# Performance work log

Hardware: AMD Instinct MI355X
Metric: run time of the kernel (lower is better)

Reference implementation:

```python
import jax, jax.numpy as jnp
import numpy as np

N_USERS = 100000
N_ITEMS = 100000
D = 64
B, P, H = 32, 1000, 128
EPS = 1e-12


def setup_inputs() -> dict:
    key = jax.random.key(0)
    ks = jax.random.split(key, 9)
    user_index = jax.random.randint(ks[0], (B,), 0, N_USERS)
    pred_item_indices = jax.random.randint(ks[1], (B, P), 0, N_ITEMS)
    history_item_indices = jax.random.randint(ks[2], (B, H), 0, N_ITEMS)
    # positive listen-time gaps (seconds-scale)
    history_timedeltas = jax.random.uniform(ks[3], (B, H), jnp.float32) * 100.0
    history_weights = jnp.ones((B, H), jnp.float32)
    embedding_user = jax.random.normal(ks[4], (N_USERS + 1, D), jnp.float32) * 0.1
    embedding_item = jax.random.normal(ks[5], (N_ITEMS + 1, D), jnp.float32) * 0.1
    user_lamb = jax.random.normal(ks[6], (N_USERS + 1, 1), jnp.float32) * 0.01
    user_bias = jax.random.normal(ks[7], (N_USERS + 1, 1), jnp.float32) * 0.01
    item_bias = jax.random.normal(ks[8], (N_ITEMS + 1, 1), jnp.float32) * 0.01
    return {
        'user_index': user_index,
        'pred_item_indices': pred_item_indices,
        'history_item_indices': history_item_indices,
        'history_timedeltas': history_timedeltas,
        'history_weights': history_weights,
        'embedding_user': embedding_user,
        'embedding_item': embedding_item,
        'user_lamb': user_lamb,
        'user_bias': user_bias,
        'item_bias': item_bias,
        'global_lamb': jnp.float32(1.0),
        'alpha': jnp.float32(1.0),
        'beta': jnp.float32(-0.065),
        'gamma': jnp.float32(0.5),
        'cutoff': jnp.float32(3.0),
        'smooth': jnp.float32(1.0),
        'force': jnp.float32(1.0),
    }


def reference(user_index, pred_item_indices, history_item_indices,
              history_timedeltas, history_weights,
              embedding_user, embedding_item, user_lamb, user_bias, item_bias,
              global_lamb, alpha, beta, gamma, cutoff, smooth, force):
    u = embedding_user[user_index][:, None, :]              # [B,1,D]
    p = embedding_item[pred_item_indices]                   # [B,P,D]
    dist_ui = jnp.sqrt(jnp.sum((u - p) ** 2, axis=2) + EPS)  # [B,P]

    h = embedding_item[history_item_indices]                # [B,H,D]
    # pairwise L2 via Gram trick: avoids the [B,H,P,D] broadcast intermediate
    sq = (jnp.sum(h * h, -1)[:, :, None]
          + jnp.sum(p * p, -1)[:, None, :]
          - 2.0 * jnp.einsum('bhd,bpd->bhp', h, p))         # [B,H,P]
    dist = jnp.sqrt(jnp.maximum(sq, 0.0) + EPS)

    denom = jax.nn.sigmoid(smooth - force * smooth)
    kern = jax.nn.sigmoid(smooth / (1.0 + dist) - force * smooth) / denom  # [B,H,P]

    td = (history_timedeltas + cutoff) ** (-0.5) * history_weights  # [B,H]
    lamb = global_lamb + user_lamb[user_index]              # [B,1]
    res = lamb * jnp.einsum('bh,bhp->bp', td, kern)         # [B,P]

    out = jnp.maximum(0.0, dist_ui - res)                   # [B,P]
    I = (alpha * out + beta * out ** 2 + gamma
         + user_bias[user_index]                            # [B,1] broadcast
         + item_bias[pred_item_indices][..., 0])            # [B,P]
    return I
```

## Files before the change

kernel.cpp:

```cpp
#include <hip/hip_runtime.h>
#include <hip/hip_bf16.h>

#define EPS 1e-12f

constexpr int B = 32, P = 1000, H = 128, D = 64;
constexpr int PT = 128;
constexpr int TILB = 8;
constexpr int NT = 512;

typedef __attribute__((ext_vector_type(8))) short bf16x8;
typedef __attribute__((ext_vector_type(4))) float f32x4;

__device__ __forceinline__ float fast_rcp(float x)  { return __builtin_amdgcn_rcpf(x); }
__device__ __forceinline__ float fast_sqrt(float x) { return __builtin_amdgcn_sqrtf(x); }

__device__ __forceinline__ int pk2(float x, float y) {
    union { __hip_bfloat162 t; int i; } u;
    u.t = __float22bfloat162_rn(make_float2(x, y));
    return u.i;
}
__device__ __forceinline__ bf16x8 cvt8(f32x4 a, f32x4 b) {
    union { bf16x8 v; int i[4]; } u;
    u.i[0] = pk2(a.x, a.y); u.i[1] = pk2(a.z, a.w);
    u.i[2] = pk2(b.x, b.y); u.i[3] = pk2(b.z, b.w);
    return u.v;
}
__device__ __forceinline__ f32x4 scale4(f32x4 v, float s) {
    f32x4 r; r.x = v.x * s; r.y = v.y * s; r.z = v.z * s; r.w = v.w * s;
    return r;
}
__device__ __forceinline__ float sumsq16(f32x4 a, f32x4 b, f32x4 c, f32x4 d) {
    return (a.x*a.x + a.y*a.y + a.z*a.z + a.w*a.w)
         + (b.x*b.x + b.y*b.y + b.z*b.z + b.w*b.w)
         + (c.x*c.x + c.y*c.y + c.z*c.z + c.w*c.w)
         + (d.x*d.x + d.y*d.y + d.z*d.z + d.w*d.w);
}

__device__ __forceinline__ int swz(int row, int kg) { return kg ^ ((row >> 1) & 3); }

__global__ __launch_bounds__(NT, 2)
void ex2vec_kernel(const int* __restrict__ user_index,
                   const int* __restrict__ pred_items,
                   const int* __restrict__ hist_items,
                   const float* __restrict__ hist_td,
                   const float* __restrict__ hist_w,
                   const float* __restrict__ emb_user,
                   const float* __restrict__ emb_item,
                   const float* __restrict__ user_lamb,
                   const float* __restrict__ user_bias,
                   const float* __restrict__ item_bias,
                   const float* __restrict__ sc_global_lamb,
                   const float* __restrict__ sc_alpha,
                   const float* __restrict__ sc_beta,
                   const float* __restrict__ sc_gamma,
                   const float* __restrict__ sc_cutoff,
                   const float* __restrict__ sc_smooth,
                   const float* __restrict__ sc_force,
                   float* __restrict__ out)
{
    __shared__ bf16x8 afs[2][H][4];
    __shared__ float  hh[H];
    __shared__ float  tds[H];

    const int b    = blockIdx.x >> 3;
    const int tile = blockIdx.x & 7;
    const int tid  = threadIdx.x;
    const int w    = tid >> 6;
    const int lane = tid & 63;
    const int col  = lane & 15;
    const int kg   = lane >> 4;

    const int pg   = tile * PT + w * 16 + col;
    const int pgc  = pg < P ? pg : P - 1;
    const int pidx = pred_items[b * P + pgc];

    const float* prow = emb_item + (size_t)pidx * D + kg * 8;
    const f32x4 p0 = *(const f32x4*)(prow);
    const f32x4 p1 = *(const f32x4*)(prow + 4);
    const f32x4 p2 = *(const f32x4*)(prow + 32);
    const f32x4 p3 = *(const f32x4*)(prow + 36);

    const float cutoff = *sc_cutoff;

    {
        const int r = tid >> 2;
        const int q = tid & 3;
        const int hidx = hist_items[b * H + r];
        const f32x4* hsrc = (const f32x4*)(emb_item + (size_t)hidx * D + q * 16);
        const f32x4 v0 = hsrc[0], v1 = hsrc[1], v2 = hsrc[2], v3 = hsrc[3];

        float s = sumsq16(v0, v1, v2, v3);
        s += __shfl_xor(s, 1);
        s += __shfl_xor(s, 2);
        if (q == 0) {
            hh[r]  = s;
            tds[r] = hist_w[b * H + r] * __frsqrt_rn(hist_td[b * H + r] + cutoff);
        }
        afs[q >> 1][r][swz(r, (q & 1) * 2)]     = cvt8(v0, v1);
        afs[q >> 1][r][swz(r, (q & 1) * 2 + 1)] = cvt8(v2, v3);
    }

    float pp = sumsq16(p0, p1, p2, p3);
    pp += __shfl_xor(pp, 16);
    pp += __shfl_xor(pp, 32);
    const bf16x8 bfr0 = cvt8(scale4(p0, -2.f), scale4(p1, -2.f));
    const bf16x8 bfr1 = cvt8(scale4(p2, -2.f), scale4(p3, -2.f));

    const float smooth = *sc_smooth;
    const float fs     = *sc_force * smooth;

    __syncthreads();

    float pres = 0.f;
    #pragma unroll
    for (int t = 0; t < 8; ++t) {
        const int row = t * 16 + col;
        const bf16x8 af0 = afs[0][row][swz(row, kg)];
        const bf16x8 af1 = afs[1][row][swz(row, kg)];
        const f32x4  hh4 = *(const f32x4*)(hh  + t * 16 + kg * 4);
        const f32x4  td4 = *(const f32x4*)(tds + t * 16 + kg * 4);

        f32x4 acc;
        acc.x = pp + hh4[0]; acc.y = pp + hh4[1];
        acc.z = pp + hh4[2]; acc.w = pp + hh4[3];
        acc = __builtin_amdgcn_mfma_f32_16x16x32_bf16(af0, bfr0, acc, 0, 0, 0);
        acc = __builtin_amdgcn_mfma_f32_16x16x32_bf16(af1, bfr1, acc, 0, 0, 0);

        #pragma unroll
        for (int j = 0; j < 4; ++j) {
            const float dist = fast_sqrt(fmaxf(acc[j], 0.f) + EPS);
            const float x    = smooth * fast_rcp(1.f + dist) - fs;
            pres += td4[j] * fast_rcp(1.f + __expf(-x));
        }
    }
    pres += __shfl_xor(pres, 16);
    pres += __shfl_xor(pres, 32);

    const int uidx = user_index[b];
    const float* urow = emb_user + (size_t)uidx * D + kg * 8;
    f32x4 d0 = *(const f32x4*)(urow)      - p0;
    f32x4 d1 = *(const f32x4*)(urow + 4)  - p1;
    f32x4 d2 = *(const f32x4*)(urow + 32) - p2;
    f32x4 d3 = *(const f32x4*)(urow + 36) - p3;
    float dp = sumsq16(d0, d1, d2, d3);
    dp += __shfl_xor(dp, 16);
    dp += __shfl_xor(dp, 32);

    if (lane < 16 && pg < P) {
        const float inv_denom = 1.f + __expf(fs - smooth);
        const float lamb      = (*sc_global_lamb + user_lamb[uidx]) * inv_denom;
        const float dist_ui   = fast_sqrt(dp + EPS);
        const float o = fmaxf(0.f, dist_ui - lamb * pres);
        out[b * P + pg] = (*sc_alpha) * o + (*sc_beta) * o * o + (*sc_gamma)
                          + user_bias[uidx] + item_bias[pidx];
    }
}

extern "C" void kernel_launch(void* const* d_in, const int* in_sizes, int n_in,
                              void* d_out, int out_size, void* d_ws, size_t ws_size,
                              hipStream_t stream) {
    (void)in_sizes; (void)n_in; (void)d_ws; (void)ws_size; (void)out_size;
    ex2vec_kernel<<<dim3(B * TILB), dim3(NT), 0, stream>>>(
        (const int*)d_in[0],  (const int*)d_in[1],  (const int*)d_in[2],
        (const float*)d_in[3], (const float*)d_in[4],
        (const float*)d_in[5], (const float*)d_in[6],
        (const float*)d_in[7], (const float*)d_in[8], (const float*)d_in[9],
        (const float*)d_in[10], (const float*)d_in[11], (const float*)d_in[12],
        (const float*)d_in[13], (const float*)d_in[14], (const float*)d_in[15],
        (const float*)d_in[16], (float*)d_out);
}
```

Baseline: 11.06 us.

## Split history staging into two halves to overlap gather with MFMA compute

History embeddings are now staged in two halves of 64 rows, with each thread loading 8 floats per row instead of 16. The second half's global loads are issued before the first half's MFMA and sigmoid loop, and written to shared memory only after that loop, so gather latency overlaps with compute. The block-to-(batch, tile) mapping is also changed so consecutive blocks cover different batches. This adds a second barrier and keeps more registers live across the first compute loop.

```diff
diff --git a/kernel.cpp b/kernel.cpp
--- a/kernel.cpp
+++ b/kernel.cpp
@@ -5,7 +5,6 @@
 
 constexpr int B = 32, P = 1000, H = 128, D = 64;
 constexpr int PT = 128;
-constexpr int TILB = 8;
 constexpr int NT = 512;
 
 typedef __attribute__((ext_vector_type(8))) short bf16x8;
@@ -29,11 +28,12 @@
     f32x4 r; r.x = v.x * s; r.y = v.y * s; r.z = v.z * s; r.w = v.w * s;
     return r;
 }
+__device__ __forceinline__ float sumsq8(f32x4 a, f32x4 b) {
+    return (a.x*a.x + a.y*a.y + a.z*a.z + a.w*a.w)
+         + (b.x*b.x + b.y*b.y + b.z*b.z + b.w*b.w);
+}
 __device__ __forceinline__ float sumsq16(f32x4 a, f32x4 b, f32x4 c, f32x4 d) {
-    return (a.x*a.x + a.y*a.y + a.z*a.z + a.w*a.w)
-         + (b.x*b.x + b.y*b.y + b.z*b.z + b.w*b.w)
-         + (c.x*c.x + c.y*c.y + c.z*c.z + c.w*c.w)
-         + (d.x*d.x + d.y*d.y + d.z*d.z + d.w*d.w);
+    return sumsq8(a, b) + sumsq8(c, d);
 }
 
 __device__ __forceinline__ int swz(int row, int kg) { return kg ^ ((row >> 1) & 3); }
@@ -62,8 +62,8 @@
     __shared__ float  hh[H];
     __shared__ float  tds[H];
 
-    const int b    = blockIdx.x >> 3;
-    const int tile = blockIdx.x & 7;
+    const int b    = blockIdx.x & 31;
+    const int tile = blockIdx.x >> 5;
     const int tid  = threadIdx.x;
     const int w    = tid >> 6;
     const int lane = tid & 63;
@@ -82,59 +82,35 @@
 
     const float cutoff = *sc_cutoff;
 
+    const int r8 = tid >> 3;
+    const int e  = tid & 7;
+    const int rA = r8;
+    const int rB = 64 + r8;
+
     {
-        const int r = tid >> 2;
-        const int q = tid & 3;
-        const int hidx = hist_items[b * H + r];
-        const f32x4* hsrc = (const f32x4*)(emb_item + (size_t)hidx * D + q * 16);
-        const f32x4 v0 = hsrc[0], v1 = hsrc[1], v2 = hsrc[2], v3 = hsrc[3];
-
-        float s = sumsq16(v0, v1, v2, v3);
-        s += __shfl_xor(s, 1);
-        s += __shfl_xor(s, 2);
-        if (q == 0) {
-            hh[r]  = s;
-            tds[r] = hist_w[b * H + r] * __frsqrt_rn(hist_td[b * H + r] + cutoff);
-        }
-        afs[q >> 1][r][swz(r, (q & 1) * 2)]     = cvt8(v0, v1);
-        afs[q >> 1][r][swz(r, (q & 1) * 2 + 1)] = cvt8(v2, v3);
-    }
+        const int hidx = hist_items[b * H + rA];
+        const f32x4* src = (const f32x4*)(emb_item + (size_t)hidx * D + e * 8);
+        const f32x4 v0 = src[0], v1 = src[1];
+        float s = sumsq8(v0, v1);
+        s += __shfl_xor(s, 1); s += __shfl_xor(s, 2); s += __shfl_xor(s, 4);
+        if (e == 0) {
+            hh[rA]  = s;
+            tds[rA] = hist_w[b * H + rA] * __frsqrt_rn(hist_td[b * H + rA] + cutoff);
+        }
+        afs[e >> 2][rA][swz(rA, e & 3)] = cvt8(v0, v1);
+    }
+
+    const int hidxB = hist_items[b * H + rB];
+    const f32x4* srcB = (const f32x4*)(emb_item + (size_t)hidxB * D + e * 8);
+    const f32x4 b0 = srcB[0], b1 = srcB[1];
+    const float wB = hist_w[b * H + rB];
+    const float tB = hist_td[b * H + rB];
 
     float pp = sumsq16(p0, p1, p2, p3);
     pp += __shfl_xor(pp, 16);
     pp += __shfl_xor(pp, 32);
     const bf16x8 bfr0 = cvt8(scale4(p0, -2.f), scale4(p1, -2.f));
     const bf16x8 bfr1 = cvt8(scale4(p2, -2.f), scale4(p3, -2.f));
-
-    const float smooth = *sc_smooth;
-    const float fs     = *sc_force * smooth;
-
-    __syncthreads();
-
-    float pres = 0.f;
-    #pragma unroll
-    for (int t = 0; t < 8; ++t) {
-        const int row = t * 16 + col;
-        const bf16x8 af0 = afs[0][row][swz(row, kg)];
-        const bf16x8 af1 = afs[1][row][swz(row, kg)];
-        const f32x4  hh4 = *(const f32x4*)(hh  + t * 16 + kg * 4);
-        const f32x4  td4 = *(const f32x4*)(tds + t * 16 + kg * 4);
-
-        f32x4 acc;
-        acc.x = pp + hh4[0]; acc.y = pp + hh4[1];
-        acc.z = pp + hh4[2]; acc.w = pp + hh4[3];
-        acc = __builtin_amdgcn_mfma_f32_16x16x32_bf16(af0, bfr0, acc, 0, 0, 0);
-        acc = __builtin_amdgcn_mfma_f32_16x16x32_bf16(af1, bfr1, acc, 0, 0, 0);
-
-        #pragma unroll
-        for (int j = 0; j < 4; ++j) {
-            const float dist = fast_sqrt(fmaxf(acc[j], 0.f) + EPS);
-            const float x    = smooth * fast_rcp(1.f + dist) - fs;
-            pres += td4[j] * fast_rcp(1.f + __expf(-x));
-        }
-    }
-    pres += __shfl_xor(pres, 16);
-    pres += __shfl_xor(pres, 32);
 
     const int uidx = user_index[b];
     const float* urow = emb_user + (size_t)uidx * D + kg * 8;
@@ -146,6 +122,69 @@
     dp += __shfl_xor(dp, 16);
     dp += __shfl_xor(dp, 32);
 
+    const float smooth = *sc_smooth;
+    const float fs     = *sc_force * smooth;
+
+    __syncthreads();
+
+    float pres = 0.f;
+    #pragma unroll
+    for (int t = 0; t < 4; ++t) {
+        const int row = t * 16 + col;
+        const bf16x8 af0 = afs[0][row][swz(row, kg)];
+        const bf16x8 af1 = afs[1][row][swz(row, kg)];
+        const f32x4  hh4 = *(const f32x4*)(hh  + t * 16 + kg * 4);
+        const f32x4  td4 = *(const f32x4*)(tds + t * 16 + kg * 4);
+
+        f32x4 acc;
+        acc.x = pp + hh4[0]; acc.y = pp + hh4[1];
+        acc.z = pp + hh4[2]; acc.w = pp + hh4[3];
+        acc = __builtin_amdgcn_mfma_f32_16x16x32_bf16(af0, bfr0, acc, 0, 0, 0);
+        acc = __builtin_amdgcn_mfma_f32_16x16x32_bf16(af1, bfr1, acc, 0, 0, 0);
+
+        #pragma unroll
+        for (int j = 0; j < 4; ++j) {
+            const float dist = fast_sqrt(fmaxf(acc[j], 0.f) + EPS);
+            const float x    = smooth * fast_rcp(1.f + dist) - fs;
+            pres += td4[j] * fast_rcp(1.f + __expf(-x));
+        }
+    }
+
+    {
+        float s = sumsq8(b0, b1);
+        s += __shfl_xor(s, 1); s += __shfl_xor(s, 2); s += __shfl_xor(s, 4);
+        if (e == 0) {
+            hh[rB]  = s;
+            tds[rB] = wB * __frsqrt_rn(tB + cutoff);
+        }
+        afs[e >> 2][rB][swz(rB, e & 3)] = cvt8(b0, b1);
+    }
+    __syncthreads();
+
+    #pragma unroll
+    for (int t = 4; t < 8; ++t) {
+        const int row = t * 16 + col;
+        const bf16x8 af0 = afs[0][row][swz(row, kg)];
+        const bf16x8 af1 = afs[1][row][swz(row, kg)];
+        const f32x4  hh4 = *(const f32x4*)(hh  + t * 16 + kg * 4);
+        const f32x4  td4 = *(const f32x4*)(tds + t * 16 + kg * 4);
+
+        f32x4 acc;
+        acc.x = pp + hh4[0]; acc.y = pp + hh4[1];
+        acc.z = pp + hh4[2]; acc.w = pp + hh4[3];
+        acc = __builtin_amdgcn_mfma_f32_16x16x32_bf16(af0, bfr0, acc, 0, 0, 0);
+        acc = __builtin_amdgcn_mfma_f32_16x16x32_bf16(af1, bfr1, acc, 0, 0, 0);
+
+        #pragma unroll
+        for (int j = 0; j < 4; ++j) {
+            const float dist = fast_sqrt(fmaxf(acc[j], 0.f) + EPS);
+            const float x    = smooth * fast_rcp(1.f + dist) - fs;
+            pres += td4[j] * fast_rcp(1.f + __expf(-x));
+        }
+    }
+    pres += __shfl_xor(pres, 16);
+    pres += __shfl_xor(pres, 32);
+
     if (lane < 16 && pg < P) {
         const float inv_denom = 1.f + __expf(fs - smooth);
         const float lamb      = (*sc_global_lamb + user_lamb[uidx]) * inv_denom;
@@ -160,7 +199,7 @@
                               void* d_out, int out_size, void* d_ws, size_t ws_size,
                               hipStream_t stream) {
     (void)in_sizes; (void)n_in; (void)d_ws; (void)ws_size; (void)out_size;
-    ex2vec_kernel<<<dim3(B * TILB), dim3(NT), 0, stream>>>(
+    ex2vec_kernel<<<dim3(B * 8), dim3(NT), 0, stream>>>(
         (const int*)d_in[0],  (const int*)d_in[1],  (const int*)d_in[2],
         (const float*)d_in[3], (const float*)d_in[4],
         (const float*)d_in[5], (const float*)d_in[6],
```

Result: slower. 12.20 us, median of 2 (+10.3%).
